# Optimization experiments

Hardware: AMD Instinct MI355X
Metric: run time of the kernel (lower is better)

## Reference

```python
import math
import jax, jax.numpy as jnp
import numpy as np
from jax import lax

SQRT2 = 1.4142135623730951
EPS = 1e-8


def _make_kernel():
    k = jnp.array([1.0, 3.0, 3.0, 1.0], jnp.float32)
    k = k[None, :] * k[:, None]
    return k / k.sum()  # [4,4], sums to 1


def _blur(x, kernel, pad, up=1):
    # upfirdn2d: optional zero-insertion upsample, pad, FIR filter (depthwise conv)
    C = x.shape[1]
    rhs = jnp.broadcast_to(kernel[None, None], (C, 1, kernel.shape[0], kernel.shape[1]))
    p0, p1 = pad
    if up > 1:
        p1 = p1 + (up - 1)  # zero-insertion appends up-1 trailing zeros per axis
    return lax.conv_general_dilated(
        x, rhs, (1, 1), [(p0, p1), (p0, p1)], lhs_dilation=(up, up),
        dimension_numbers=('NCHW', 'OIHW', 'NCHW'), feature_group_count=C)


def _mod_linear(style, mw, mb):
    # EqualLinear: scale = 1/sqrt(in_dim)
    scale = 1.0 / math.sqrt(mw.shape[1])
    return style @ (mw * scale).T + mb


def _mod_weight(w, s, demodulate):
    # w: [O,I,kh,kw], s: [B,I] -> per-sample weights [B,O,I,kh,kw]
    scale = 1.0 / math.sqrt(w.shape[1] * w.shape[2] * w.shape[3])
    wb = scale * w[None] * s[:, None, :, None, None]
    if demodulate:
        d = lax.rsqrt(jnp.sum(wb * wb, axis=(2, 3, 4)) + EPS)
        wb = wb * d[:, :, None, None, None]
    return wb


def _per_sample_conv(x, wb, padding):
    def f(xi, wi):
        return lax.conv_general_dilated(
            xi[None], wi, (1, 1), [(padding, padding)] * 2,
            dimension_numbers=('NCHW', 'OIHW', 'NCHW'))[0]
    return jax.vmap(f)(x, wb)


def _per_sample_conv_transpose2(x, wb):
    # torch conv_transpose2d(stride=2, pad=0) == lhs-dilated conv with flipped kernel
    k = wb.shape[-1]
    def f(xi, wi):
        return lax.conv_general_dilated(
            xi[None], jnp.flip(wi, (2, 3)), (1, 1), [(k - 1, k - 1)] * 2,
            lhs_dilation=(2, 2), dimension_numbers=('NCHW', 'OIHW', 'NCHW'))[0]
    return jax.vmap(f)(x, wb)


def _fused_lrelu(x, b):
    return jax.nn.leaky_relu(x + b[None, :, None, None], 0.2) * SQRT2


def setup_inputs() -> dict:
    key = jax.random.key(0)
    ks = jax.random.split(key, 16)
    B, C, H, S = 8, 512, 32, 512
    return {
        'x': jax.random.normal(ks[0], (B, C, H, H), jnp.float32),
        'style': jax.random.normal(ks[1], (B, S), jnp.float32),
        'skip_rgb': jax.random.normal(ks[2], (B, 3, H, H), jnp.float32),
        'noise1': jax.random.normal(ks[3], (B, 1, 2 * H, 2 * H), jnp.float32),
        'noise2': jax.random.normal(ks[4], (B, 1, 2 * H, 2 * H), jnp.float32),
        'w1': jax.random.normal(ks[5], (C, C, 3, 3), jnp.float32),
        'mod1_w': jax.random.normal(ks[6], (C, S), jnp.float32),
        'mod1_b': jnp.ones((C,), jnp.float32),
        'bias1': jnp.zeros((C,), jnp.float32),
        'noise1_w': 0.1 * jnp.ones((1,), jnp.float32),
        'w2': jax.random.normal(ks[7], (C, C, 3, 3), jnp.float32),
        'mod2_w': jax.random.normal(ks[8], (C, S), jnp.float32),
        'mod2_b': jnp.ones((C,), jnp.float32),
        'bias2': jnp.zeros((C,), jnp.float32),
        'noise2_w': 0.1 * jnp.ones((1,), jnp.float32),
        'w3': jax.random.normal(ks[9], (3, C, 1, 1), jnp.float32),
        'mod3_w': jax.random.normal(ks[10], (C, S), jnp.float32),
        'mod3_b': jnp.ones((C,), jnp.float32),
        'bias3': jnp.zeros((3,), jnp.float32),
    }


def reference(x, style, skip_rgb, noise1, noise2,
              w1, mod1_w, mod1_b, bias1, noise1_w,
              w2, mod2_w, mod2_b, bias2, noise2_w,
              w3, mod3_w, mod3_b, bias3):
    kernel = _make_kernel()
    # --- StyledConv with upsample: modulated conv_transpose + blur + noise + fused lrelu
    s1 = _mod_linear(style, mod1_w, mod1_b)            # [B, Cin]
    wb1 = _mod_weight(w1, s1, True)                    # [B, O, I, 3, 3]
    out = _per_sample_conv_transpose2(x, wb1)          # [B, O, 2H+1, 2W+1]
    out = _blur(out, kernel * 4.0, (1, 1))             # [B, O, 2H, 2W]
    out = out + noise1_w[0] * noise1
    out = _fused_lrelu(out, bias1)
    # --- StyledConv, same resolution
    s2 = _mod_linear(style, mod2_w, mod2_b)
    wb2 = _mod_weight(w2, s2, True)
    out = _per_sample_conv(out, wb2, 1)
    out = out + noise2_w[0] * noise2
    out = _fused_lrelu(out, bias2)
    # --- ToRGB: 1x1 modulated conv (no demodulation) + bias + upsampled skip
    s3 = _mod_linear(style, mod3_w, mod3_b)
    wb3 = _mod_weight(w3, s3, False)
    rgb = _per_sample_conv(out, wb3, 0) + bias3[None, :, None, None]
    skip = _blur(skip_rgb, kernel * 4.0, (2, 1), up=2)  # Upsample(factor=2)
    return rgb + skip
```

## Files before the change

kernel.cpp:

```cpp
#include <hip/hip_runtime.h>

typedef _Float16 f16;
typedef __attribute__((ext_vector_type(4))) _Float16 f16x4;
typedef __attribute__((ext_vector_type(8))) _Float16 f16x8;
typedef __attribute__((ext_vector_type(4))) float f32x4;

#define SC_CONV 0.014731391274719738f
#define SC_RGB  0.04419417382415922f
#define SC_LIN  0.04419417382415922f
#define SQRT2F  1.4142135623730951f

__device__ inline f32x4 zero_f32x4() {
    f32x4 v;
    #pragma unroll
    for (int i = 0; i < 4; ++i) v[i] = 0.0f;
    return v;
}
__device__ inline void gload_lds16(const void* g, void* l) {
    __builtin_amdgcn_global_load_lds(
        (const __attribute__((address_space(1))) unsigned int*)g,
        (__attribute__((address_space(3))) unsigned int*)l, 16, 0, 0);
}

__global__ __launch_bounds__(256) void k_prep1(
    const float* __restrict__ style,
    const float* __restrict__ m1w, const float* __restrict__ m1b,
    const float* __restrict__ m2w, const float* __restrict__ m2b,
    const float* __restrict__ m3w, const float* __restrict__ m3b,
    float* __restrict__ s1, float* __restrict__ s2, float* __restrict__ s3,
    const float* __restrict__ w1, const float* __restrict__ w2,
    f16* __restrict__ wA1, f16* __restrict__ wA2,
    f16* __restrict__ xmh, f16* __restrict__ in1h, f16* __restrict__ ctp,
    const float* __restrict__ skiprgb, const float* __restrict__ bias3,
    float* __restrict__ out)
{
    const int bx = blockIdx.x;
    if (bx < 2048) {
        int g = bx * 256 + threadIdx.x;
        int set = g >> 18; int oi = g & 262143;
        const float* w = (set ? w2 : w1) + (size_t)oi * 9;
        f16* wa = set ? wA2 : wA1;
        int o = oi >> 9, i = oi & 511;
        #pragma unroll
        for (int t = 0; t < 9; ++t)
            wa[((size_t)t * 512 + o) * 512 + i] = (f16)w[t];
    } else if (bx < 2432) {
        const int lane = threadIdx.x & 63, wid = threadIdx.x >> 6;
        const int gw = (bx - 2048) * 4 + wid;
        const int set = gw >> 9, o = gw & 511;
        const float* mw = set == 0 ? m1w : set == 1 ? m2w : m3w;
        const float* mb = set == 0 ? m1b : set == 1 ? m2b : m3b;
        float* outp = set == 0 ? s1 : set == 1 ? s2 : s3;
        const float4 m0 = *(const float4*)(mw + (size_t)o * 512 + lane * 8);
        const float4 m1 = *(const float4*)(mw + (size_t)o * 512 + lane * 8 + 4);
        const float mv[8] = {m0.x, m0.y, m0.z, m0.w, m1.x, m1.y, m1.z, m1.w};
        float acc[8];
        #pragma unroll
        for (int b = 0; b < 8; ++b) {
            const float4 sA = *(const float4*)(style + b * 512 + lane * 8);
            const float4 sB = *(const float4*)(style + b * 512 + lane * 8 + 4);
            acc[b] = mv[0]*sA.x + mv[1]*sA.y + mv[2]*sA.z + mv[3]*sA.w
                   + mv[4]*sB.x + mv[5]*sB.y + mv[6]*sB.z + mv[7]*sB.w;
        }
        #pragma unroll
        for (int b = 0; b < 8; ++b)
            #pragma unroll
            for (int off = 1; off < 64; off <<= 1)
                acc[b] += __shfl_xor(acc[b], off);
        if (lane == 0) {
            const float mbv = mb[o];
            #pragma unroll
            for (int b = 0; b < 8; ++b) outp[b * 512 + o] = acc[b] * SC_LIN + mbv;
        }
    } else if (bx < 2448) {
        const int idx = bx - 2432, b = idx & 7, type = idx >> 3;
        f16x8 z;
        #pragma unroll
        for (int i = 0; i < 8; ++i) z[i] = (_Float16)0.0f;
        if (type == 0) {
            for (int j = threadIdx.x; j < 132 * 64; j += 256) {
                int pix = j >> 6, e = j & 63;
                int r, c;
                if (pix < 34)       { r = 0;            c = pix; }
                else if (pix < 68)  { r = 33;           c = pix - 34; }
                else if (pix < 100) { r = pix - 68 + 1; c = 0; }
                else                { r = pix - 100 + 1; c = 33; }
                *(f16x8*)(xmh + ((((size_t)b * 34 + r) * 34 + c) * 512) + e * 8) = z;
            }
        } else {
            for (int j = threadIdx.x; j < 260 * 64; j += 256) {
                int pix = j >> 6, e = j & 63;
                int r, c;
                if (pix < 66)       { r = 0;             c = pix; }
                else if (pix < 132) { r = 65;            c = pix - 66; }
                else if (pix < 196) { r = pix - 132 + 1; c = 0; }
                else                { r = pix - 196 + 1; c = 65; }
                *(f16x8*)(in1h + ((((size_t)b * 66 + r) * 66 + c) * 512) + e * 8) = z;
            }
        }
    } else if (bx < 2456) {
        const int b = bx - 2448;
        f16x8 z;
        #pragma unroll
        for (int i = 0; i < 8; ++i) z[i] = (_Float16)0.0f;
        for (int j = threadIdx.x; j < 266 * 64; j += 256) {
            int pix = j >> 6, e = j & 63;
            int r, c;
            if (pix < 68)       { r = 0;             c = pix; }
            else if (pix < 136) { r = 66;            c = pix - 68; }
            else if (pix < 201) { r = 1 + (pix - 136); c = 0; }
            else                { r = 1 + (pix - 201); c = 66; }
            *(f16x8*)(ctp + ((((size_t)b * 68 + r) * 68 + c) * 512) + e * 8) = z;
        }
    } else {
        const unsigned g = (unsigned)(bx - 2456) * 256 + threadIdx.x;
        const unsigned b = g / 12288u, rem = g - b * 12288u;
        const unsigned c = rem >> 12, pix = rem & 4095u;
        const int y = (int)(pix >> 6), xx = (int)(pix & 63);
        const float kk[4] = {1.f, 3.f, 3.f, 1.f};
        int sy = y & 1, sx = xx & 1;
        int u0 = ((y + sy) >> 1) - 1, v0 = ((xx + sx) >> 1) - 1;
        float cy0 = kk[sy], cy1 = kk[sy + 2], cx0 = kk[sx], cx1 = kk[sx + 2];
        float sk = 0.f;
        #pragma unroll
        for (int aa = 0; aa < 2; ++aa)
            #pragma unroll
            for (int bb = 0; bb < 2; ++bb) {
                int u = u0 + aa, vv = v0 + bb;
                if (u >= 0 && u < 32 && vv >= 0 && vv < 32)
                    sk += (aa ? cy1 : cy0) * (bb ? cx1 : cx0) *
                          skiprgb[(((size_t)b * 3 + c) * 32 + u) * 32 + vv];
            }
        out[(((size_t)b * 3 + c) * 64 + y) * 64 + xx] = bias3[c] + sk * (1.0f / 16.0f);
    }
}

__global__ __launch_bounds__(256) void k_prep2(
    const float* __restrict__ w1, const float* __restrict__ s1, float* __restrict__ d1,
    const float* __restrict__ w2, const float* __restrict__ s2, float* __restrict__ d2,
    const float* __restrict__ x, f16* __restrict__ xmh)
{
    __shared__ float red[8][4];
    __shared__ float t[32][33];
    const int bx = blockIdx.x;
    if (bx < 1024) {
        const int o = bx & 511, set = bx >> 9;
        const float* w = set ? w2 : w1;
        const float* s = set ? s2 : s1;
        float* d = set ? d2 : d1;
        float acc[8] = {0,0,0,0,0,0,0,0};
        for (int i = threadIdx.x; i < 512; i += 256) {
            const float* wp = w + ((size_t)o * 512 + i) * 9;
            float sw = 0.f;
            #pragma unroll
            for (int tt = 0; tt < 9; ++tt) { float vv = wp[tt]; sw += vv * vv; }
            #pragma unroll
            for (int b = 0; b < 8; ++b) { float sv = s[b * 512 + i]; acc[b] += sv * sv * sw; }
        }
        const int lane = threadIdx.x & 63, wid = threadIdx.x >> 6;
        #pragma unroll
        for (int b = 0; b < 8; ++b)
            #pragma unroll
            for (int off = 1; off < 64; off <<= 1)
                acc[b] += __shfl_xor(acc[b], off);
        if (lane == 0) {
            #pragma unroll
            for (int b = 0; b < 8; ++b) red[b][wid] = acc[b];
        }
        __syncthreads();
        if (threadIdx.x < 8) {
            float s4 = red[threadIdx.x][0] + red[threadIdx.x][1] + red[threadIdx.x][2] + red[threadIdx.x][3];
            d[threadIdx.x * 512 + o] = rsqrtf(s4 * (SC_CONV * SC_CONV) + 1e-8f);
        }
    } else {
        const int idx = bx - 1024, u = idx & 31, b = idx >> 5;
        int tx = threadIdx.x & 31, ty = threadIdx.x >> 5;
        for (int ic = 0; ic < 512; ic += 32) {
            #pragma unroll
            for (int k = 0; k < 4; ++k) {
                int i = ic + ty + 8 * k;
                t[ty + 8 * k][tx] = x[(((size_t)b * 512 + i) * 32 + u) * 32 + tx];
            }
            __syncthreads();
            #pragma unroll
            for (int k = 0; k < 4; ++k) {
                int v = ty + 8 * k;
                int i = ic + tx;
                float sv = s1[b * 512 + i] * SC_CONV;
                xmh[(((size_t)b * 34 + u + 1) * 34 + v + 1) * 512 + i] = (f16)(t[tx][v] * sv);
            }
            __syncthreads();
        }
    }
}

__global__ __launch_bounds__(512, 2) void k_conv1m(
    const f16* __restrict__ xmh, const f16* __restrict__ wA1, f16* __restrict__ ctp)
{
    const int gid = blockIdx.x;
    int ph, tbase;
    if (gid < 70)       { ph = 0; tbase = 0; }
    else if (gid < 136) { ph = 1; tbase = 70; }
    else if (gid < 202) { ph = 2; tbase = 136; }
    else                { ph = 3; tbase = 202; }
    const int p = ph >> 1, q = ph & 1;
    const int Nn = q ? 32 : 33;
    const unsigned npos = (unsigned)((p ? 32 : 33) * Nn);
    const unsigned ntot = npos * 8;
    const int tiles_n = (int)((ntot + 255) >> 8);
    int t = gid - tbase;
    const int mB = (t >= tiles_n) ? 256 : 0;
    if (t >= tiles_n) t -= tiles_n;
    const unsigned posB = (unsigned)t * 256;
    const int ntx = q ? 1 : 2;
    const int ntaps = (p ? 1 : 2) * ntx;
    const int ktsteps = ntaps * 8;

    __shared__ f16 LA[2][16384];
    __shared__ f16 LB[2][16384];
    const int tid = threadIdx.x, lane = tid & 63, wid = tid >> 6;
    const int wm = wid >> 2, wn = wid & 3;
    const int lr = lane & 15, lk = lane >> 4;

    f32x4 acc[8][4];
    #pragma unroll
    for (int mf = 0; mf < 8; ++mf)
        #pragma unroll
        for (int nf = 0; nf < 4; ++nf) acc[mf][nf] = zero_f32x4();

    int aoff[4], boff[4], ldst[4];
    #pragma unroll
    for (int c = 0; c < 4; ++c) {
        const int idx = c * 512 + tid;
        const int row = idx >> 3, sl = idx & 7, ssl = sl ^ (row & 7);
        ldst[c] = idx * 16;
        aoff[c] = (mB + row) * 512 + ssl * 8;
        unsigned pos = posB + (unsigned)row;
        if (pos > ntot - 1) pos = ntot - 1;
        const unsigned bb = pos / npos, rr = pos - bb * npos;
        const unsigned u = rr / (unsigned)Nn, v = rr - u * (unsigned)Nn;
        boff[c] = (int)(((bb * 34 + u + 1) * 34 + v + 1) * 512) + ssl * 8;
    }

    int raA[8], raB[4];
    #pragma unroll
    for (int mf = 0; mf < 8; ++mf) {
        const int R = wm * 128 + mf * 16 + lr;
        raA[mf] = R * 128 + ((lk ^ (R & 7)) * 16);
    }
    #pragma unroll
    for (int nf = 0; nf < 4; ++nf) {
        const int R = wn * 64 + nf * 16 + lr;
        raB[nf] = R * 128 + ((lk ^ (R & 7)) * 16);
    }

    auto stageA = [&](int kt, int d) {
        const int tt = kt >> 3, icb = (kt & 7) << 6;
        const int ay = (ntx == 2) ? (tt >> 1) : tt;
        const int ax = (ntx == 2) ? (tt & 1) : 0;
        const f16* base = wA1 + (size_t)((p + 2 * ay) * 3 + (q + 2 * ax)) * 262144 + icb;
        char* dst = (char*)LA[d];
        #pragma unroll
        for (int c = 0; c < 4; ++c)
            gload_lds16(base + aoff[c], dst + ldst[c]);
    };
    auto stageB = [&](int kt, int d) {
        const int tt = kt >> 3, icb = (kt & 7) << 6;
        const int ay = (ntx == 2) ? (tt >> 1) : tt;
        const int ax = (ntx == 2) ? (tt & 1) : 0;
        const f16* base = xmh - (long)(ay * 34 + ax) * 512 + icb;
        char* dst = (char*)LB[d];
        #pragma unroll
        for (int c = 0; c < 4; ++c)
            gload_lds16(base + boff[c], dst + ldst[c]);
    };

    stageB(0, 0);
    stageA(0, 0);
    for (int kt = 0; kt < ktsteps; ++kt) {
        const int d = kt & 1;
        asm volatile("s_waitcnt vmcnt(0)" ::: "memory");
        __builtin_amdgcn_s_barrier();
        const char* A = (const char*)LA[d];
        const char* Bm = (const char*)LB[d];
        f16x8 bf[4][2], af[4][2];
        #pragma unroll
        for (int nf = 0; nf < 4; ++nf) {
            bf[nf][0] = *(const f16x8*)(Bm + raB[nf]);
            bf[nf][1] = *(const f16x8*)(Bm + (raB[nf] ^ 64));
        }
        #pragma unroll
        for (int mf = 0; mf < 4; ++mf) {
            af[mf][0] = *(const f16x8*)(A + raA[mf]);
            af[mf][1] = *(const f16x8*)(A + (raA[mf] ^ 64));
        }
        if (kt + 1 < ktsteps) stageB(kt + 1, d ^ 1);
        asm volatile("s_waitcnt lgkmcnt(0)" ::: "memory");
        __builtin_amdgcn_sched_barrier(0);
        __builtin_amdgcn_s_setprio(1);
        #pragma unroll
        for (int mf = 0; mf < 4; ++mf)
            #pragma unroll
            for (int nf = 0; nf < 4; ++nf) {
                acc[mf][nf] = __builtin_amdgcn_mfma_f32_16x16x32_f16(
                    af[mf][0], bf[nf][0], acc[mf][nf], 0, 0, 0);
                acc[mf][nf] = __builtin_amdgcn_mfma_f32_16x16x32_f16(
                    af[mf][1], bf[nf][1], acc[mf][nf], 0, 0, 0);
            }
        __builtin_amdgcn_s_setprio(0);
        #pragma unroll
        for (int mf = 0; mf < 4; ++mf) {
            af[mf][0] = *(const f16x8*)(A + raA[mf + 4]);
            af[mf][1] = *(const f16x8*)(A + (raA[mf + 4] ^ 64));
        }
        if (kt + 1 < ktsteps) stageA(kt + 1, d ^ 1);
        asm volatile("s_waitcnt lgkmcnt(0)" ::: "memory");
        __builtin_amdgcn_sched_barrier(0);
        __builtin_amdgcn_s_setprio(1);
        #pragma unroll
        for (int mf = 0; mf < 4; ++mf)
            #pragma unroll
            for (int nf = 0; nf < 4; ++nf) {
                acc[mf + 4][nf] = __builtin_amdgcn_mfma_f32_16x16x32_f16(
                    af[mf][0], bf[nf][0], acc[mf + 4][nf], 0, 0, 0);
                acc[mf + 4][nf] = __builtin_amdgcn_mfma_f32_16x16x32_f16(
                    af[mf][1], bf[nf][1], acc[mf + 4][nf], 0, 0, 0);
            }
        __builtin_amdgcn_s_setprio(0);
    }

    #pragma unroll
    for (int nf = 0; nf < 4; ++nf) {
        const int c = wn * 64 + nf * 16 + lr;
        const unsigned pos = posB + (unsigned)c;
        if (pos >= ntot) continue;
        const unsigned bb = pos / npos, rr = pos - bb * npos;
        const unsigned u = rr / (unsigned)Nn, v = rr - u * (unsigned)Nn;
        const int row = 1 + 2 * (int)u + p, col = 1 + 2 * (int)v + q;
        f16* dst = ctp + (((size_t)bb * 68 + row) * 68 + col) * 512;
        #pragma unroll
        for (int mf = 0; mf < 8; ++mf) {
            const int ob = mB + wm * 128 + mf * 16 + lk * 4;
            f16x4 st;
            #pragma unroll
            for (int r = 0; r < 4; ++r) st[r] = (f16)acc[mf][nf][r];
            *(f16x4*)(dst + ob) = st;
        }
    }
}

__global__ __launch_bounds__(256) void k_blur1(
    const f16* __restrict__ ctp, const float* __restrict__ d1,
    const float* __restrict__ noise1, const float* __restrict__ nw1,
    const float* __restrict__ bias1, const float* __restrict__ s2,
    f16* __restrict__ in1h)
{
    const int y0 = blockIdx.x * 2, b = blockIdx.y;
    const int tx = threadIdx.x & 63, xg = threadIdx.x >> 6;
    const int ch = tx * 8, x0 = xg * 16;
    const f16* base = ctp + ((size_t)(b * 68 + y0) * 68) * 512 + ch;

    float d1v[8], b1v[8], s2v[8];
    {
        const float4 a0 = *(const float4*)(d1 + b * 512 + ch);
        const float4 a1 = *(const float4*)(d1 + b * 512 + ch + 4);
        const float4 c0 = *(const float4*)(bias1 + ch);
        const float4 c1 = *(const float4*)(bias1 + ch + 4);
        const float4 e0 = *(const float4*)(s2 + b * 512 + ch);
        const float4 e1 = *(const float4*)(s2 + b * 512 + ch + 4);
        d1v[0]=a0.x; d1v[1]=a0.y; d1v[2]=a0.z; d1v[3]=a0.w;
        d1v[4]=a1.x; d1v[5]=a1.y; d1v[6]=a1.z; d1v[7]=a1.w;
        b1v[0]=c0.x; b1v[1]=c0.y; b1v[2]=c0.z; b1v[3]=c0.w;
        b1v[4]=c1.x; b1v[5]=c1.y; b1v[6]=c1.z; b1v[7]=c1.w;
        s2v[0]=e0.x; s2v[1]=e0.y; s2v[2]=e0.z; s2v[3]=e0.w;
        s2v[4]=e1.x; s2v[5]=e1.y; s2v[6]=e1.z; s2v[7]=e1.w;
    }
    const float nw = nw1[0];
    const float* nrow0 = noise1 + ((size_t)b * 64 + y0) * 64;
    const float* nrow1 = nrow0 + 64;

    float cs[4][2][8];
    #define LOADCOL(cc, slot)                                                   \
        do {                                                                    \
            f16x8 v0 = *(const f16x8*)(base + ((size_t)(0 * 68 + (cc))) * 512); \
            f16x8 v1 = *(const f16x8*)(base + ((size_t)(1 * 68 + (cc))) * 512); \
            f16x8 v2 = *(const f16x8*)(base + ((size_t)(2 * 68 + (cc))) * 512); \
            f16x8 v3 = *(const f16x8*)(base + ((size_t)(3 * 68 + (cc))) * 512); \
            f16x8 v4 = *(const f16x8*)(base + ((size_t)(4 * 68 + (cc))) * 512); \
            _Pragma("unroll")                                                   \
            for (int k = 0; k < 8; ++k) {                                       \
                float f0=(float)v0[k], f1=(float)v1[k], f2=(float)v2[k];        \
                float f3=(float)v3[k], f4=(float)v4[k];                         \
                cs[slot][0][k] = f0 + 3.f*f1 + 3.f*f2 + f3;                     \
                cs[slot][1][k] = f1 + 3.f*f2 + 3.f*f3 + f4;                     \
            }                                                                   \
        } while (0)

    LOADCOL(x0 + 0, 0);
    LOADCOL(x0 + 1, 1);
    LOADCOL(x0 + 2, 2);
    #pragma unroll
    for (int xi = 0; xi < 16; ++xi) {
        LOADCOL(x0 + xi + 3, ((xi + 3) & 3));
        const int x = x0 + xi;
        const float nz0 = nw * nrow0[x];
        const float nz1 = nw * nrow1[x];
        f16x8 st0, st1;
        #pragma unroll
        for (int k = 0; k < 8; ++k) {
            float s0 = (cs[xi & 3][0][k] + cs[(xi + 3) & 3][0][k])
                     + 3.f * (cs[(xi + 1) & 3][0][k] + cs[(xi + 2) & 3][0][k]);
            float v0 = s0 * (1.0f / 16.0f) * d1v[k] + nz0 + b1v[k];
            v0 = (v0 > 0.f ? v0 : 0.2f * v0) * SQRT2F;
            st0[k] = (f16)(v0 * s2v[k] * SC_CONV);
            float s1r = (cs[xi & 3][1][k] + cs[(xi + 3) & 3][1][k])
                      + 3.f * (cs[(xi + 1) & 3][1][k] + cs[(xi + 2) & 3][1][k]);
            float v1 = s1r * (1.0f / 16.0f) * d1v[k] + nz1 + b1v[k];
            v1 = (v1 > 0.f ? v1 : 0.2f * v1) * SQRT2F;
            st1[k] = (f16)(v1 * s2v[k] * SC_CONV);
        }
        *(f16x8*)(in1h + (((size_t)(b * 66 + 1 + y0) * 66) + 1 + x) * 512 + ch) = st0;
        *(f16x8*)(in1h + (((size_t)(b * 66 + 2 + y0) * 66) + 1 + x) * 512 + ch) = st1;
    }
    #undef LOADCOL
}

__global__ __launch_bounds__(512, 2) void k_conv2_8p(
    const f16* __restrict__ in1h, const f16* __restrict__ wA2,
    const float* __restrict__ d2, const float* __restrict__ noise2,
    const float* __restrict__ nw2, const float* __restrict__ bias2,
    const float* __restrict__ s3, const float* __restrict__ w3,
    float* __restrict__ out)
{
    const int b = blockIdx.z, mB = blockIdx.y * 256, nT = blockIdx.x;
    const int y0 = nT * 4;
    __shared__ f16 LA[2][16384];
    __shared__ f16 LB[2][16384];
    const int tid = threadIdx.x, lane = tid & 63, wid = tid >> 6;
    const int wm = wid >> 2, wn = wid & 3;
    const int lr = lane & 15, lk = lane >> 4;

    f32x4 acc[8][4];
    #pragma unroll
    for (int mf = 0; mf < 8; ++mf)
        #pragma unroll
        for (int nf = 0; nf < 4; ++nf) acc[mf][nf] = zero_f32x4();

    int aoff[4], boff[4], ldst[4];
    #pragma unroll
    for (int c = 0; c < 4; ++c) {
        const int idx = c * 512 + tid;
        const int row = idx >> 3, sl = idx & 7, ssl = sl ^ (row & 7);
        ldst[c] = idx * 16;
        aoff[c] = (mB + row) * 512 + ssl * 8;
        const int py = y0 + (row >> 6), px = row & 63;
        boff[c] = ((b * 66 + 1 + py) * 66 + 1 + px) * 512 + ssl * 8;
    }

    int raA[8], raB[4];
    #pragma unroll
    for (int mf = 0; mf < 8; ++mf) {
        const int R = wm * 128 + mf * 16 + lr;
        raA[mf] = R * 128 + ((lk ^ (R & 7)) * 16);
    }
    #pragma unroll
    for (int nf = 0; nf < 4; ++nf) {
        const int R = wn * 64 + nf * 16 + lr;
        raB[nf] = R * 128 + ((lk ^ (R & 7)) * 16);
    }

    auto stageA = [&](int kt, int d) {
        const int tap = kt >> 3, icb = (kt & 7) << 6;
        const f16* base = wA2 + (size_t)tap * 262144 + icb;
        char* dst = (char*)LA[d];
        #pragma unroll
        for (int c = 0; c < 4; ++c)
            gload_lds16(base + aoff[c], dst + ldst[c]);
    };
    auto stageB = [&](int kt, int d) {
        const int tap = kt >> 3, icb = (kt & 7) << 6;
        const int dy = tap / 3 - 1, dx = tap - (tap / 3) * 3 - 1;
        const f16* base = in1h + (dy * 66 + dx) * 512 + icb;
        char* dst = (char*)LB[d];
        #pragma unroll
        for (int c = 0; c < 4; ++c)
            gload_lds16(base + boff[c], dst + ldst[c]);
    };

    stageB(0, 0);
    stageA(0, 0);
    for (int kt = 0; kt < 72; ++kt) {
        const int d = kt & 1;
        asm volatile("s_waitcnt vmcnt(0)" ::: "memory");
        __builtin_amdgcn_s_barrier();
        const char* A = (const char*)LA[d];
        const char* Bm = (const char*)LB[d];
        f16x8 bf[4][2], af[4][2];
        #pragma unroll
        for (int nf = 0; nf < 4; ++nf) {
            bf[nf][0] = *(const f16x8*)(Bm + raB[nf]);
            bf[nf][1] = *(const f16x8*)(Bm + (raB[nf] ^ 64));
        }
        #pragma unroll
        for (int mf = 0; mf < 4; ++mf) {
            af[mf][0] = *(const f16x8*)(A + raA[mf]);
            af[mf][1] = *(const f16x8*)(A + (raA[mf] ^ 64));
        }
        if (kt + 1 < 72) stageB(kt + 1, d ^ 1);
        asm volatile("s_waitcnt lgkmcnt(0)" ::: "memory");
        __builtin_amdgcn_sched_barrier(0);
        __builtin_amdgcn_s_setprio(1);
        #pragma unroll
        for (int mf = 0; mf < 4; ++mf)
            #pragma unroll
            for (int nf = 0; nf < 4; ++nf) {
                acc[mf][nf] = __builtin_amdgcn_mfma_f32_16x16x32_f16(
                    af[mf][0], bf[nf][0], acc[mf][nf], 0, 0, 0);
                acc[mf][nf] = __builtin_amdgcn_mfma_f32_16x16x32_f16(
                    af[mf][1], bf[nf][1], acc[mf][nf], 0, 0, 0);
            }
        __builtin_amdgcn_s_setprio(0);
        #pragma unroll
        for (int mf = 0; mf < 4; ++mf) {
            af[mf][0] = *(const f16x8*)(A + raA[mf + 4]);
            af[mf][1] = *(const f16x8*)(A + (raA[mf + 4] ^ 64));
        }
        if (kt + 1 < 72) stageA(kt + 1, d ^ 1);
        asm volatile("s_waitcnt lgkmcnt(0)" ::: "memory");
        __builtin_amdgcn_sched_barrier(0);
        __builtin_amdgcn_s_setprio(1);
        #pragma unroll
        for (int mf = 0; mf < 4; ++mf)
            #pragma unroll
            for (int nf = 0; nf < 4; ++nf) {
                acc[mf + 4][nf] = __builtin_amdgcn_mfma_f32_16x16x32_f16(
                    af[mf][0], bf[nf][0], acc[mf + 4][nf], 0, 0, 0);
                acc[mf + 4][nf] = __builtin_amdgcn_mfma_f32_16x16x32_f16(
                    af[mf][1], bf[nf][1], acc[mf + 4][nf], 0, 0, 0);
            }
        __builtin_amdgcn_s_setprio(0);
    }

    const float* d2b = d2 + b * 512;
    const float* s3b = s3 + b * 512;
    const float nw = nw2[0];
    float p3[4][3];
    #pragma unroll
    for (int nf = 0; nf < 4; ++nf)
        #pragma unroll
        for (int c = 0; c < 3; ++c) p3[nf][c] = 0.f;
    #pragma unroll
    for (int mf = 0; mf < 8; ++mf) {
        const int ob = mB + wm * 128 + mf * 16 + lk * 4;
        const float4 dv = *(const float4*)(d2b + ob);
        const float4 bv = *(const float4*)(bias2 + ob);
        const float4 sv = *(const float4*)(s3b + ob);
        const float4 w0 = *(const float4*)(w3 + 0 * 512 + ob);
        const float4 w1v = *(const float4*)(w3 + 1 * 512 + ob);
        const float4 w2v = *(const float4*)(w3 + 2 * 512 + ob);
        const float dd[4] = {dv.x, dv.y, dv.z, dv.w};
        const float bb[4] = {bv.x, bv.y, bv.z, bv.w};
        const float ss[4] = {sv.x, sv.y, sv.z, sv.w};
        const float w0r[4] = {w0.x, w0.y, w0.z, w0.w};
        const float w1r[4] = {w1v.x, w1v.y, w1v.z, w1v.w};
        const float w2r[4] = {w2v.x, w2v.y, w2v.z, w2v.w};
        #pragma unroll
        for (int nf = 0; nf < 4; ++nf) {
            const int c = wn * 64 + nf * 16 + lr;
            const int py = y0 + (c >> 6), px = c & 63;
            const float nz = nw * noise2[((size_t)b * 64 + py) * 64 + px];
            #pragma unroll
            for (int r = 0; r < 4; ++r) {
                float v = acc[mf][nf][r] * dd[r] + nz + bb[r];
                v = (v > 0.f ? v : 0.2f * v) * SQRT2F;
                v *= ss[r] * SC_RGB;
                p3[nf][0] += v * w0r[r];
                p3[nf][1] += v * w1r[r];
                p3[nf][2] += v * w2r[r];
            }
        }
    }
    #pragma unroll
    for (int nf = 0; nf < 4; ++nf)
        #pragma unroll
        for (int c = 0; c < 3; ++c) {
            float v = p3[nf][c];
            v += __shfl_xor(v, 16);
            v += __shfl_xor(v, 32);
            p3[nf][c] = v;
        }
    if (lk == 0) {
        #pragma unroll
        for (int nf = 0; nf < 4; ++nf) {
            const int c = wn * 64 + nf * 16 + lr;
            const int py = y0 + (c >> 6), px = c & 63;
            #pragma unroll
            for (int ch = 0; ch < 3; ++ch)
                atomicAdd(out + (((size_t)b * 3 + ch) * 64 + py) * 64 + px, p3[nf][ch]);
        }
    }
}

extern "C" void kernel_launch(void* const* d_in, const int* in_sizes, int n_in,
                              void* d_out, int out_size, void* d_ws, size_t ws_size,
                              hipStream_t stream)
{
    const float* x       = (const float*)d_in[0];
    const float* style   = (const float*)d_in[1];
    const float* skiprgb = (const float*)d_in[2];
    const float* noise1  = (const float*)d_in[3];
    const float* noise2  = (const float*)d_in[4];
    const float* w1      = (const float*)d_in[5];
    const float* m1w     = (const float*)d_in[6];
    const float* m1b     = (const float*)d_in[7];
    const float* bias1   = (const float*)d_in[8];
    const float* nw1     = (const float*)d_in[9];
    const float* w2      = (const float*)d_in[10];
    const float* m2w     = (const float*)d_in[11];
    const float* m2b     = (const float*)d_in[12];
    const float* bias2   = (const float*)d_in[13];
    const float* nw2     = (const float*)d_in[14];
    const float* w3      = (const float*)d_in[15];
    const float* m3w     = (const float*)d_in[16];
    const float* m3b     = (const float*)d_in[17];
    const float* bias3   = (const float*)d_in[18];
    float* out = (float*)d_out;

    char* p = (char*)d_ws;
    auto alloc = [&](size_t bytes) { char* r = p; p += (bytes + 255) & ~(size_t)255; return r; };
    float* s1 = (float*)alloc(8 * 512 * 4);
    float* s2 = (float*)alloc(8 * 512 * 4);
    float* s3 = (float*)alloc(8 * 512 * 4);
    float* d1 = (float*)alloc(8 * 512 * 4);
    float* d2 = (float*)alloc(8 * 512 * 4);
    f16* wA1 = (f16*)alloc((size_t)9 * 512 * 512 * 2);
    f16* wA2 = (f16*)alloc((size_t)9 * 512 * 512 * 2);
    const size_t XMH_B  = (size_t)8 * 34 * 34 * 512 * 2;
    const size_t CTP_B  = (size_t)8 * 68 * 68 * 512 * 2;
    const size_t IN1H_B = (size_t)8 * 66 * 66 * 512 * 2;
    char* ovl = (char*)alloc(XMH_B + CTP_B + IN1H_B);
    f16* xmh  = (f16*)ovl;
    f16* ctp  = (f16*)(ovl + XMH_B);
    f16* in1h = (f16*)(ovl + XMH_B + CTP_B);

    k_prep1<<<2840, 256, 0, stream>>>(style, m1w, m1b, m2w, m2b, m3w, m3b, s1, s2, s3,
                                      w1, w2, wA1, wA2, xmh, in1h, ctp,
                                      skiprgb, bias3, out);
    k_prep2<<<1280, 256, 0, stream>>>(w1, s1, d1, w2, s2, d2, x, xmh);
    k_conv1m<<<266, 512, 0, stream>>>(xmh, wA1, ctp);
    k_blur1<<<dim3(32, 8), 256, 0, stream>>>(ctp, d1, noise1, nw1, bias1, s2, in1h);
    k_conv2_8p<<<dim3(16, 2, 8), 512, 0, stream>>>(in1h, wA2, d2, noise2, nw2, bias2, s3, w3, out);
}
```

Before: 248.3 us.

## Precompute weight square sums, issue both stage loads early, remap conv2 grid

k_prep1 now computes per-(o,i) sums of squared 3x3 weights while converting weights to f16, so k_prep2 reads one float instead of re-reading nine weights for demodulation. In both GEMM conv kernels the A-tile global-to-LDS prefetch is issued together with the B-tile prefetch at the start of the iteration rather than midway, giving loads more time to land before the next barrier. The conv2 launch becomes a flat 1D grid with the batch index in the low bits, which changes block scheduling order and likely L2 reuse of weights across batches. The costs are extra workspace for the square sums and more outstanding memory traffic early in each iteration.

```diff
diff --git a/kernel.cpp b/kernel.cpp
--- a/kernel.cpp
+++ b/kernel.cpp
@@ -30,6 +30,7 @@
     float* __restrict__ s1, float* __restrict__ s2, float* __restrict__ s3,
     const float* __restrict__ w1, const float* __restrict__ w2,
     f16* __restrict__ wA1, f16* __restrict__ wA2,
+    float* __restrict__ wsq1, float* __restrict__ wsq2,
     f16* __restrict__ xmh, f16* __restrict__ in1h, f16* __restrict__ ctp,
     const float* __restrict__ skiprgb, const float* __restrict__ bias3,
     float* __restrict__ out)
@@ -40,10 +41,16 @@
         int set = g >> 18; int oi = g & 262143;
         const float* w = (set ? w2 : w1) + (size_t)oi * 9;
         f16* wa = set ? wA2 : wA1;
+        float* wq = set ? wsq2 : wsq1;
         int o = oi >> 9, i = oi & 511;
-        #pragma unroll
-        for (int t = 0; t < 9; ++t)
-            wa[((size_t)t * 512 + o) * 512 + i] = (f16)w[t];
+        float sw = 0.f;
+        #pragma unroll
+        for (int t = 0; t < 9; ++t) {
+            float v = w[t];
+            wa[((size_t)t * 512 + o) * 512 + i] = (f16)v;
+            sw += v * v;
+        }
+        wq[oi] = sw;
     } else if (bx < 2432) {
         const int lane = threadIdx.x & 63, wid = threadIdx.x >> 6;
         const int gw = (bx - 2048) * 4 + wid;
@@ -136,8 +143,8 @@
 }
 
 __global__ __launch_bounds__(256) void k_prep2(
-    const float* __restrict__ w1, const float* __restrict__ s1, float* __restrict__ d1,
-    const float* __restrict__ w2, const float* __restrict__ s2, float* __restrict__ d2,
+    const float* __restrict__ wsq1, const float* __restrict__ s1, float* __restrict__ d1,
+    const float* __restrict__ wsq2, const float* __restrict__ s2, float* __restrict__ d2,
     const float* __restrict__ x, f16* __restrict__ xmh)
 {
     __shared__ float red[8][4];
@@ -145,15 +152,12 @@
     const int bx = blockIdx.x;
     if (bx < 1024) {
         const int o = bx & 511, set = bx >> 9;
-        const float* w = set ? w2 : w1;
+        const float* wq = set ? wsq2 : wsq1;
         const float* s = set ? s2 : s1;
         float* d = set ? d2 : d1;
         float acc[8] = {0,0,0,0,0,0,0,0};
         for (int i = threadIdx.x; i < 512; i += 256) {
-            const float* wp = w + ((size_t)o * 512 + i) * 9;
-            float sw = 0.f;
-            #pragma unroll
-            for (int tt = 0; tt < 9; ++tt) { float vv = wp[tt]; sw += vv * vv; }
+            const float sw = wq[(size_t)o * 512 + i];
             #pragma unroll
             for (int b = 0; b < 8; ++b) { float sv = s[b * 512 + i]; acc[b] += sv * sv * sw; }
         }
@@ -294,7 +298,7 @@
             af[mf][0] = *(const f16x8*)(A + raA[mf]);
             af[mf][1] = *(const f16x8*)(A + (raA[mf] ^ 64));
         }
-        if (kt + 1 < ktsteps) stageB(kt + 1, d ^ 1);
+        if (kt + 1 < ktsteps) { stageB(kt + 1, d ^ 1); stageA(kt + 1, d ^ 1); }
         asm volatile("s_waitcnt lgkmcnt(0)" ::: "memory");
         __builtin_amdgcn_sched_barrier(0);
         __builtin_amdgcn_s_setprio(1);
@@ -313,7 +317,6 @@
             af[mf][0] = *(const f16x8*)(A + raA[mf + 4]);
             af[mf][1] = *(const f16x8*)(A + (raA[mf + 4] ^ 64));
         }
-        if (kt + 1 < ktsteps) stageA(kt + 1, d ^ 1);
         asm volatile("s_waitcnt lgkmcnt(0)" ::: "memory");
         __builtin_amdgcn_sched_barrier(0);
         __builtin_amdgcn_s_setprio(1);
@@ -432,7 +435,9 @@
     const float* __restrict__ s3, const float* __restrict__ w3,
     float* __restrict__ out)
 {
-    const int b = blockIdx.z, mB = blockIdx.y * 256, nT = blockIdx.x;
+    const int bid = blockIdx.x;
+    const int b = bid & 7, tt0 = bid >> 3;
+    const int mB = (tt0 & 1) << 8, nT = tt0 >> 1;
     const int y0 = nT * 4;
     __shared__ f16 LA[2][16384];
     __shared__ f16 LB[2][16384];
@@ -506,7 +511,7 @@
             af[mf][0] = *(const f16x8*)(A + raA[mf]);
             af[mf][1] = *(const f16x8*)(A + (raA[mf] ^ 64));
         }
-        if (kt + 1 < 72) stageB(kt + 1, d ^ 1);
+        if (kt + 1 < 72) { stageB(kt + 1, d ^ 1); stageA(kt + 1, d ^ 1); }
         asm volatile("s_waitcnt lgkmcnt(0)" ::: "memory");
         __builtin_amdgcn_sched_barrier(0);
         __builtin_amdgcn_s_setprio(1);
@@ -525,7 +530,6 @@
             af[mf][0] = *(const f16x8*)(A + raA[mf + 4]);
             af[mf][1] = *(const f16x8*)(A + (raA[mf + 4] ^ 64));
         }
-        if (kt + 1 < 72) stageA(kt + 1, d ^ 1);
         asm volatile("s_waitcnt lgkmcnt(0)" ::: "memory");
         __builtin_amdgcn_sched_barrier(0);
         __builtin_amdgcn_s_setprio(1);
@@ -633,6 +637,8 @@
     float* s3 = (float*)alloc(8 * 512 * 4);
     float* d1 = (float*)alloc(8 * 512 * 4);
     float* d2 = (float*)alloc(8 * 512 * 4);
+    float* wsq1 = (float*)alloc((size_t)512 * 512 * 4);
+    float* wsq2 = (float*)alloc((size_t)512 * 512 * 4);
     f16* wA1 = (f16*)alloc((size_t)9 * 512 * 512 * 2);
     f16* wA2 = (f16*)alloc((size_t)9 * 512 * 512 * 2);
     const size_t XMH_B  = (size_t)8 * 34 * 34 * 512 * 2;
@@ -644,10 +650,10 @@
     f16* in1h = (f16*)(ovl + XMH_B + CTP_B);
 
     k_prep1<<<2840, 256, 0, stream>>>(style, m1w, m1b, m2w, m2b, m3w, m3b, s1, s2, s3,
-                                      w1, w2, wA1, wA2, xmh, in1h, ctp,
+                                      w1, w2, wA1, wA2, wsq1, wsq2, xmh, in1h, ctp,
                                       skiprgb, bias3, out);
-    k_prep2<<<1280, 256, 0, stream>>>(w1, s1, d1, w2, s2, d2, x, xmh);
+    k_prep2<<<1280, 256, 0, stream>>>(wsq1, s1, d1, wsq2, s2, d2, x, xmh);
     k_conv1m<<<266, 512, 0, stream>>>(xmh, wA1, ctp);
     k_blur1<<<dim3(32, 8), 256, 0, stream>>>(ctp, d1, noise1, nw1, bias1, s2, in1h);
-    k_conv2_8p<<<dim3(16, 2, 8), 512, 0, stream>>>(in1h, wA2, d2, noise2, nw2, bias2, s3, w3, out);
-}
+    k_conv2_8p<<<256, 512, 0, stream>>>(in1h, wA2, d2, noise2, nw2, bias2, s3, w3, out);
+}
```

After: 248.8 us. About the same (+0.2%).
